# Kernel tuning notes

Hardware: AMD Instinct MI355X
Metric: run time of the kernel (lower is better)

## Reference

```python
import jax, jax.numpy as jnp
import numpy as np

SEQ = 64  # hard-coded by tf.tile multiples=[1, 64, 1]


def setup_inputs() -> dict:
    key = jax.random.key(0)
    k1, k2, k3, k4 = jax.random.split(key, 4)
    B, V, D = 1024, 300, 512
    return {
        "word_ids_en": jax.random.randint(k1, (B, SEQ), 0, V, dtype=jnp.int32),
        "word_ids_fr": jax.random.randint(k2, (B, SEQ), 0, V, dtype=jnp.int32),
        "emb_kernel": jax.random.normal(k3, (V, D), dtype=jnp.float32) * 0.05,
        "Qdense": jax.random.normal(k4, (D, D), dtype=jnp.float32) * 0.05,
    }


def reference(word_ids_en, word_ids_fr, emb_kernel, Qdense):
    # Encoder side (French)
    embedded_fr = emb_kernel[word_ids_fr]                      # [B, S, D]
    mask_fr = (word_ids_fr != 0).astype(jnp.float32)           # [B, S]
    # Q = K = V = x @ W (same weight, three identical projections in source)
    qkv = jnp.einsum('bsd,de->bse', embedded_fr, Qdense)       # [B, S, D]
    # scores = Q K^T, masked multiplicatively along the key axis (no softmax)
    scores = jnp.einsum('bqd,bkd->bqk', qkv, qkv) * mask_fr[:, None, :]  # [B, S, S]
    encoded = jnp.einsum('bqk,bkd->bqd', scores, qkv)          # [B, S, D]
    # Decoder side (English) + residual add
    embedded_en = emb_kernel[word_ids_en]                      # [B, S, D]
    return embedded_en + encoded
```

## Files before the change

### kernel.cpp

```cpp
#include <hip/hip_runtime.h>
#include <hip/hip_bf16.h>

#define SEQ 64
#define DIM 512
#define VOCAB 300
#define LDQ 516
#define LDSC 72

typedef __attribute__((ext_vector_type(8))) short short8;
typedef __attribute__((ext_vector_type(4))) float floatx4;

static __device__ inline unsigned short f2bf(float x) {
    __hip_bfloat16 t = __float2bfloat16(x);
    return *reinterpret_cast<unsigned short*>(&t);
}

static __device__ inline short8 ld8(const unsigned short* p) {
    union { short8 s; uint2 u[2]; } r;
    r.u[0] = *(const uint2*)p;
    r.u[1] = *(const uint2*)(p + 4);
    return r.s;
}

__global__ __launch_bounds__(64) void proj_kernel(
    const float* __restrict__ emb,
    const float* __restrict__ Q,
    __hip_bfloat16* __restrict__ P)
{
    const int lane = threadIdx.x & 63;
    const int quad = lane >> 4;
    const int l16 = lane & 15;
    const int nt = blockIdx.x;
    const int mt = blockIdx.y;
    const int n = nt * 16 + l16;
    const int vrow = mt * 16 + l16;

    floatx4 acc = {};
#pragma unroll 4
    for (int k0 = 0; k0 < DIM; k0 += 32) {
        float4 x0 = {0, 0, 0, 0}, x1 = {0, 0, 0, 0};
        if (vrow < VOCAB) {
            x0 = *(const float4*)(emb + (size_t)vrow * DIM + k0 + quad * 8);
            x1 = *(const float4*)(emb + (size_t)vrow * DIM + k0 + quad * 8 + 4);
        }
        union { short8 s; unsigned short h[8]; } ua;
        ua.h[0] = f2bf(x0.x); ua.h[1] = f2bf(x0.y); ua.h[2] = f2bf(x0.z); ua.h[3] = f2bf(x0.w);
        ua.h[4] = f2bf(x1.x); ua.h[5] = f2bf(x1.y); ua.h[6] = f2bf(x1.z); ua.h[7] = f2bf(x1.w);

        union { short8 s; unsigned short h[8]; } ub;
#pragma unroll
        for (int j = 0; j < 8; j++)
            ub.h[j] = f2bf(Q[(size_t)(k0 + quad * 8 + j) * DIM + n]);

        acc = __builtin_amdgcn_mfma_f32_16x16x32_bf16(ua.s, ub.s, acc, 0, 0, 0);
    }
#pragma unroll
    for (int r = 0; r < 4; r++) {
        int v = mt * 16 + quad * 4 + r;
        if (v < VOCAB) P[(size_t)v * DIM + n] = __float2bfloat16(acc[r]);
    }
}

__global__ __launch_bounds__(512, 4) void fused_attn_kernel(
    const int* __restrict__ ids_en,
    const int* __restrict__ ids_fr,
    const float* __restrict__ emb,
    const __hip_bfloat16* __restrict__ P,
    float* __restrict__ out)
{
    __shared__ __align__(16) unsigned short qk[SEQ * LDQ];
    __shared__ __align__(16) unsigned short sc[SEQ * LDSC];
    __shared__ float maskS[SEQ];
    __shared__ int idsF[SEQ];
    __shared__ int idsE[SEQ];

    const int b = blockIdx.x;
    const int tid = threadIdx.x;
    const int lane = tid & 63;
    const int w = tid >> 6;
    const int quad = lane >> 4;
    const int l16 = lane & 15;
    const int n_base = w * 64;

    if (tid < SEQ) {
        int idf = ids_fr[b * SEQ + tid];
        idsF[tid] = idf;
        maskS[tid] = (idf != 0) ? 1.0f : 0.0f;
        idsE[tid] = ids_en[b * SEQ + tid];
    }
    __syncthreads();

    {
        uint4 v[8];
#pragma unroll
        for (int i = 0; i < 8; i++) {
            int c = tid + i * 512;
            v[i] = *(const uint4*)(P + (size_t)idsF[c >> 6] * DIM + (c & 63) * 8);
        }
#pragma unroll
        for (int i = 0; i < 8; i++) {
            int c = tid + i * 512;
            unsigned short* dst = qk + (c >> 6) * LDQ + (c & 63) * 8;
            *(uint2*)dst = make_uint2(v[i].x, v[i].y);
            *(uint2*)(dst + 4) = make_uint2(v[i].z, v[i].w);
        }
    }
    __syncthreads();

    short8 bbr[2][4];
    {
        floatx4 accS[2] = {};
        const int t0 = w * 2;
        const int qi = t0 >> 2;
        for (int k0 = 0; k0 < DIM; k0 += 32) {
            short8 aa = ld8(qk + (qi * 16 + l16) * LDQ + k0 + quad * 8);
#pragma unroll
            for (int i = 0; i < 2; i++) {
                int ki = (t0 + i) & 3;
                short8 bb = ld8(qk + (ki * 16 + l16) * LDQ + k0 + quad * 8);
                accS[i] = __builtin_amdgcn_mfma_f32_16x16x32_bf16(aa, bb, accS[i], 0, 0, 0);
            }
        }

#pragma unroll
        for (int kx = 0; kx < 2; kx++)
#pragma unroll
            for (int ni = 0; ni < 4; ni++)
#pragma unroll
                for (int j = 0; j < 8; j++)
                    ((unsigned short*)&bbr[kx][ni])[j] =
                        qk[(kx * 32 + quad * 8 + j) * LDQ + n_base + ni * 16 + l16];

#pragma unroll
        for (int i = 0; i < 2; i++) {
            int ki = (t0 + i) & 3;
            float m = maskS[ki * 16 + l16];
#pragma unroll
            for (int r = 0; r < 4; r++) {
                int row = qi * 16 + quad * 4 + r;
                sc[row * LDSC + ki * 16 + l16] = f2bf(accS[i][r] * m);
            }
        }
    }
    __syncthreads();

    const size_t out_base = (size_t)b * SEQ * DIM;
#pragma unroll
    for (int p = 0; p < 2; p++) {
        floatx4 acc[2][4] = {};
#pragma unroll
        for (int kx = 0; kx < 2; kx++) {
            short8 af[2];
#pragma unroll
            for (int mi = 0; mi < 2; mi++)
                af[mi] = *(const short8*)(sc + ((p * 2 + mi) * 16 + l16) * LDSC + kx * 32 + quad * 8);
#pragma unroll
            for (int ni = 0; ni < 4; ni++)
#pragma unroll
                for (int mi = 0; mi < 2; mi++)
                    acc[mi][ni] = __builtin_amdgcn_mfma_f32_16x16x32_bf16(af[mi], bbr[kx][ni], acc[mi][ni], 0, 0, 0);
        }
#pragma unroll
        for (int mi = 0; mi < 2; mi++)
#pragma unroll
            for (int ni = 0; ni < 4; ni++) {
                int col = n_base + ni * 16 + l16;
#pragma unroll
                for (int r = 0; r < 4; r++) {
                    int row = (p * 2 + mi) * 16 + quad * 4 + r;
                    float val = emb[(size_t)idsE[row] * DIM + col] + acc[mi][ni][r];
                    __builtin_nontemporal_store(val, &out[out_base + (size_t)row * DIM + col]);
                }
            }
    }
}

extern "C" void kernel_launch(void* const* d_in, const int* in_sizes, int n_in,
                              void* d_out, int out_size, void* d_ws, size_t ws_size,
                              hipStream_t stream) {
    const int* ids_en = (const int*)d_in[0];
    const int* ids_fr = (const int*)d_in[1];
    const float* emb  = (const float*)d_in[2];
    const float* Qd   = (const float*)d_in[3];
    float* out = (float*)d_out;

    const int B = in_sizes[0] / SEQ;

    __hip_bfloat16* P = (__hip_bfloat16*)d_ws;

    proj_kernel<<<dim3(32, 19), 64, 0, stream>>>(emb, Qd, P);
    fused_attn_kernel<<<B, 512, 0, stream>>>(ids_en, ids_fr, emb, P, out);
}
```

Measured before the change: 181.8 us.

## Transpose output MFMA for vectorized float4 stores and drop id staging barrier

The second matmul now swaps its MFMA operands so each lane holds four consecutive output columns. This lets the residual embedding load and the nontemporal output store use 16-byte vectors instead of scalar accesses. Token ids and mask values are read directly from global memory into registers, which removes the shared-memory staging step and one __syncthreads. The gather assigns each wave a set of rows using a readfirstlane wave index, so the row-id loads are uniform across the wave.

```diff
diff --git a/kernel.cpp b/kernel.cpp
--- a/kernel.cpp
+++ b/kernel.cpp
@@ -70,9 +70,6 @@
 {
     __shared__ __align__(16) unsigned short qk[SEQ * LDQ];
     __shared__ __align__(16) unsigned short sc[SEQ * LDSC];
-    __shared__ float maskS[SEQ];
-    __shared__ int idsF[SEQ];
-    __shared__ int idsE[SEQ];
 
     const int b = blockIdx.x;
     const int tid = threadIdx.x;
@@ -80,46 +77,46 @@
     const int w = tid >> 6;
     const int quad = lane >> 4;
     const int l16 = lane & 15;
-    const int n_base = w * 64;
-
-    if (tid < SEQ) {
-        int idf = ids_fr[b * SEQ + tid];
-        idsF[tid] = idf;
-        maskS[tid] = (idf != 0) ? 1.0f : 0.0f;
-        idsE[tid] = ids_en[b * SEQ + tid];
-    }
-    __syncthreads();
+    const int wv = __builtin_amdgcn_readfirstlane(w);
 
     {
+        int rid[8];
+#pragma unroll
+        for (int i = 0; i < 8; i++)
+            rid[i] = ids_fr[b * SEQ + i * 8 + wv];
         uint4 v[8];
 #pragma unroll
-        for (int i = 0; i < 8; i++) {
-            int c = tid + i * 512;
-            v[i] = *(const uint4*)(P + (size_t)idsF[c >> 6] * DIM + (c & 63) * 8);
-        }
+        for (int i = 0; i < 8; i++)
+            v[i] = *(const uint4*)(P + (size_t)rid[i] * DIM + lane * 8);
 #pragma unroll
         for (int i = 0; i < 8; i++) {
-            int c = tid + i * 512;
-            unsigned short* dst = qk + (c >> 6) * LDQ + (c & 63) * 8;
+            unsigned short* dst = qk + (i * 8 + wv) * LDQ + lane * 8;
             *(uint2*)dst = make_uint2(v[i].x, v[i].y);
             *(uint2*)(dst + 4) = make_uint2(v[i].z, v[i].w);
         }
     }
+
+    const int t0 = w * 2;
+    const int qi = w >> 1;
+    const int ki0 = t0 & 3, ki1 = (t0 + 1) & 3;
+    float mk0 = (ids_fr[b * SEQ + ki0 * 16 + l16] != 0) ? 1.0f : 0.0f;
+    float mk1 = (ids_fr[b * SEQ + ki1 * 16 + l16] != 0) ? 1.0f : 0.0f;
+    int idE[4];
+#pragma unroll
+    for (int q = 0; q < 4; q++)
+        idE[q] = ids_en[b * SEQ + q * 16 + l16];
+
     __syncthreads();
 
     short8 bbr[2][4];
     {
         floatx4 accS[2] = {};
-        const int t0 = w * 2;
-        const int qi = t0 >> 2;
         for (int k0 = 0; k0 < DIM; k0 += 32) {
             short8 aa = ld8(qk + (qi * 16 + l16) * LDQ + k0 + quad * 8);
-#pragma unroll
-            for (int i = 0; i < 2; i++) {
-                int ki = (t0 + i) & 3;
-                short8 bb = ld8(qk + (ki * 16 + l16) * LDQ + k0 + quad * 8);
-                accS[i] = __builtin_amdgcn_mfma_f32_16x16x32_bf16(aa, bb, accS[i], 0, 0, 0);
-            }
+            short8 b0 = ld8(qk + (ki0 * 16 + l16) * LDQ + k0 + quad * 8);
+            accS[0] = __builtin_amdgcn_mfma_f32_16x16x32_bf16(aa, b0, accS[0], 0, 0, 0);
+            short8 b1 = ld8(qk + (ki1 * 16 + l16) * LDQ + k0 + quad * 8);
+            accS[1] = __builtin_amdgcn_mfma_f32_16x16x32_bf16(aa, b1, accS[1], 0, 0, 0);
         }
 
 #pragma unroll
@@ -129,17 +126,13 @@
 #pragma unroll
                 for (int j = 0; j < 8; j++)
                     ((unsigned short*)&bbr[kx][ni])[j] =
-                        qk[(kx * 32 + quad * 8 + j) * LDQ + n_base + ni * 16 + l16];
+                        qk[(kx * 32 + quad * 8 + j) * LDQ + w * 64 + ni * 16 + l16];
 
 #pragma unroll
-        for (int i = 0; i < 2; i++) {
-            int ki = (t0 + i) & 3;
-            float m = maskS[ki * 16 + l16];
-#pragma unroll
-            for (int r = 0; r < 4; r++) {
-                int row = qi * 16 + quad * 4 + r;
-                sc[row * LDSC + ki * 16 + l16] = f2bf(accS[i][r] * m);
-            }
+        for (int r = 0; r < 4; r++) {
+            int row = qi * 16 + quad * 4 + r;
+            sc[row * LDSC + ki0 * 16 + l16] = f2bf(accS[0][r] * mk0);
+            sc[row * LDSC + ki1 * 16 + l16] = f2bf(accS[1][r] * mk1);
         }
     }
     __syncthreads();
@@ -147,31 +140,40 @@
     const size_t out_base = (size_t)b * SEQ * DIM;
 #pragma unroll
     for (int p = 0; p < 2; p++) {
+        floatx4 e[2][4];
+#pragma unroll
+        for (int mi = 0; mi < 2; mi++)
+#pragma unroll
+            for (int ni = 0; ni < 4; ni++)
+                e[mi][ni] = *(const floatx4*)(
+                    emb + (size_t)idE[p * 2 + mi] * DIM + w * 64 + ni * 16 + quad * 4);
+
         floatx4 acc[2][4] = {};
 #pragma unroll
         for (int kx = 0; kx < 2; kx++) {
-            short8 af[2];
+            short8 bf_[2];
 #pragma unroll
             for (int mi = 0; mi < 2; mi++)
-                af[mi] = *(const short8*)(sc + ((p * 2 + mi) * 16 + l16) * LDSC + kx * 32 + quad * 8);
+                bf_[mi] = *(const short8*)(
+                    sc + (p * 32 + mi * 16 + l16) * LDSC + kx * 32 + quad * 8);
 #pragma unroll
             for (int ni = 0; ni < 4; ni++)
 #pragma unroll
                 for (int mi = 0; mi < 2; mi++)
-                    acc[mi][ni] = __builtin_amdgcn_mfma_f32_16x16x32_bf16(af[mi], bbr[kx][ni], acc[mi][ni], 0, 0, 0);
+                    acc[mi][ni] = __builtin_amdgcn_mfma_f32_16x16x32_bf16(
+                        bbr[kx][ni], bf_[mi], acc[mi][ni], 0, 0, 0);
         }
+
 #pragma unroll
-        for (int mi = 0; mi < 2; mi++)
+        for (int mi = 0; mi < 2; mi++) {
+            int m = p * 32 + mi * 16 + l16;
 #pragma unroll
             for (int ni = 0; ni < 4; ni++) {
-                int col = n_base + ni * 16 + l16;
-#pragma unroll
-                for (int r = 0; r < 4; r++) {
-                    int row = (p * 2 + mi) * 16 + quad * 4 + r;
-                    float val = emb[(size_t)idsE[row] * DIM + col] + acc[mi][ni][r];
-                    __builtin_nontemporal_store(val, &out[out_base + (size_t)row * DIM + col]);
-                }
+                floatx4 o = e[mi][ni] + acc[mi][ni];
+                __builtin_nontemporal_store(
+                    o, (floatx4*)(out + out_base + (size_t)m * DIM + w * 64 + ni * 16 + quad * 4));
             }
+        }
     }
 }
 
```

Result: slower. 208.8 us (+14.8%).
